# Performance work log

Measured on AMD Instinct MI355X. Metric: run time of the kernel, lower is better.

Reference implementation:

```python
import jax, jax.numpy as jnp
import numpy as np


def setup_inputs() -> dict:
    key = jax.random.key(0)
    k1, = jax.random.split(key, 1)
    bs, A, C, H, W = 32, 3, 80, 64, 64
    inp = jax.random.normal(k1, (bs, A * (5 + C), H, W), dtype=jnp.float32)
    anchors = jnp.asarray([[116.0, 90.0], [156.0, 198.0], [373.0, 326.0]], dtype=jnp.float32)
    return {"input": inp, "anchors": anchors, "image_h": 512, "image_w": 512}


def reference(input, anchors, image_h, image_w):
    bs, ch, H, W = input.shape
    A = anchors.shape[0]
    attrs = ch // A            # 5 + num_classes
    C = attrs - 5
    stride_h = jnp.float32(image_h) / H
    stride_w = jnp.float32(image_w) / W

    # (bs, A, attrs, H, W) -> (bs, A, H, W, attrs)
    p = input.reshape(bs, A, attrs, H, W).transpose(0, 1, 3, 4, 2)

    xy = jax.nn.sigmoid(p[..., 0:2])              # (bs, A, H, W, 2)
    wh_raw = p[..., 2:4]
    conf = jax.nn.sigmoid(p[..., 4:5])
    pred_cls = jax.nn.sigmoid(p[..., 5:])

    grid_x = jnp.arange(W, dtype=jnp.float32)             # column index
    grid_y = jnp.arange(H, dtype=jnp.float32)[:, None]    # row index
    grid = jnp.stack(jnp.broadcast_arrays(grid_x, grid_y * jnp.ones((H, W), jnp.float32)), -1)
    # grid[..., 0] = grid_x, grid[..., 1] = grid_y; shape (H, W, 2)

    stride = jnp.stack([stride_w, stride_h])              # (2,)
    box_xy = (xy + grid) * stride                          # center, image coords
    box_wh = jnp.exp(wh_raw) * anchors.reshape(1, A, 1, 1, 2)  # anchors NOT scaled by stride (as in source)

    pred_boxes = jnp.concatenate([box_xy, box_wh], axis=-1)   # (bs, A, H, W, 4)

    out = jnp.concatenate(
        [pred_boxes.reshape(bs, -1, 4), conf.reshape(bs, -1, 1), pred_cls.reshape(bs, -1, C)],
        axis=-1,
    )  # (bs, A*H*W, 5+C)
    return out
```

## Files before the change

kernel.cpp:

```cpp
#include <hip/hip_runtime.h>


#define NB    32
#define NA    3
#define ATTRS 85
#define HH    64
#define WW    64
#define HWSZ  (HH * WW)
#define TPW   16
#define TILES_PER_BA (HWSZ / TPW)
#define CHUNKS (ATTRS * (TPW / 4))
#define WAVE_LDS (TPW * ATTRS)

typedef float f32x4 __attribute__((ext_vector_type(4)));

__device__ __forceinline__ float fast_sigmoid(float x) {
    return __builtin_amdgcn_rcpf(1.0f + __expf(-x));
}

__global__ __launch_bounds__(256)
void yolo_decode_kernel(const float* __restrict__ in,
                        const float* __restrict__ anchors,
                        const int* __restrict__ imh,
                        const int* __restrict__ imw,
                        float* __restrict__ out)
{
    __shared__ float lds[4 * WAVE_LDS];

    const int tid  = threadIdx.x;
    const int wid  = tid >> 6;
    const int lane = tid & 63;
    float* __restrict__ wlds = lds + wid * WAVE_LDS;

    const int wtile = blockIdx.x * 4 + wid;
    const int tile  = wtile & (TILES_PER_BA - 1);
    const int ba    = wtile >> 8;
    const int b     = ba / NA;
    const int a     = ba - b * NA;
    const int pos0  = tile * TPW;

    const float stride_w = (float)(*imw) / (float)WW;
    const float stride_h = (float)(*imh) / (float)HH;
    const float aw = anchors[a * 2 + 0];
    const float ah = anchors[a * 2 + 1];

    const float gy  = (float)(pos0 >> 6);
    const int   gx0 = pos0 & (WW - 1);

    const float* __restrict__ src =
        in + (size_t)(b * (NA * ATTRS) + a * ATTRS) * HWSZ + pos0;

    f32x4 v[6];
#pragma unroll
    for (int k = 0; k < 5; ++k) {
        const int i = k * 64 + lane;
        v[k] = *(const f32x4*)(src + (i >> 2) * HWSZ + (i & 3) * 4);
    }
    const bool tail = (lane < CHUNKS - 5 * 64);
    if (tail) {
        const int i = 5 * 64 + lane;
        v[5] = *(const f32x4*)(src + (i >> 2) * HWSZ + (i & 3) * 4);
    }

#pragma unroll
    for (int k = 0; k < 6; ++k) {
        if (k == 5 && !tail) break;
        const int i    = k * 64 + lane;
        const int attr = i >> 2;
        const int p4   = i & 3;
        float x[4] = {v[k].x, v[k].y, v[k].z, v[k].w};
        float r[4];
        if (attr >= 4) {
#pragma unroll
            for (int j = 0; j < 4; ++j)
                r[j] = fast_sigmoid(x[j]);
        } else if (attr == 0) {
#pragma unroll
            for (int j = 0; j < 4; ++j)
                r[j] = (fast_sigmoid(x[j]) + (float)(gx0 + p4 * 4 + j)) * stride_w;
        } else if (attr == 1) {
#pragma unroll
            for (int j = 0; j < 4; ++j)
                r[j] = (fast_sigmoid(x[j]) + gy) * stride_h;
        } else if (attr == 2) {
#pragma unroll
            for (int j = 0; j < 4; ++j)
                r[j] = __expf(x[j]) * aw;
        } else {
#pragma unroll
            for (int j = 0; j < 4; ++j)
                r[j] = __expf(x[j]) * ah;
        }
#pragma unroll
        for (int j = 0; j < 4; ++j)
            wlds[(p4 * 4 + j) * ATTRS + attr] = r[j];
    }

    float* __restrict__ dst =
        out + ((size_t)ba * HWSZ + pos0) * ATTRS;
#pragma unroll
    for (int k = 0; k < 5; ++k) {
        const int i = k * 64 + lane;
        *(f32x4*)(dst + i * 4) = *(const f32x4*)(wlds + i * 4);
    }
    if (tail) {
        const int i = 5 * 64 + lane;
        *(f32x4*)(dst + i * 4) = *(const f32x4*)(wlds + i * 4);
    }
}

extern "C" void kernel_launch(void* const* d_in, const int* in_sizes, int n_in,
                              void* d_out, int out_size, void* d_ws, size_t ws_size,
                              hipStream_t stream) {
    const float* in      = (const float*)d_in[0];
    const float* anchors = (const float*)d_in[1];
    const int*   imh     = (const int*)d_in[2];
    const int*   imw     = (const int*)d_in[3];
    float* out = (float*)d_out;

    const int nwaves  = NB * NA * TILES_PER_BA;
    const int nblocks = nwaves / 4;
    yolo_decode_kernel<<<nblocks, 256, 0, stream>>>(in, anchors, imh, imw, out);
}
```

Baseline: 45.43 us.

## Process a full row per wave with register double-buffered prefetch

Each wave now handles an entire 64-pixel row as four 16-pixel tiles instead of a single tile. While the current tile is decoded and written out through LDS, the loads for the next tile are issued into a second register buffer. The aim is to hide global-load latency and spread the per-wave setup over more work. In exchange the grid has a quarter as many blocks and register pressure roughly doubles, which may reduce how much memory parallelism comes from wave count.

```diff
diff --git a/kernel.cpp b/kernel.cpp
--- a/kernel.cpp
+++ b/kernel.cpp
@@ -8,7 +8,6 @@
 #define WW    64
 #define HWSZ  (HH * WW)
 #define TPW   16
-#define TILES_PER_BA (HWSZ / TPW)
 #define CHUNKS (ATTRS * (TPW / 4))
 #define WAVE_LDS (TPW * ATTRS)
 
@@ -32,80 +31,100 @@
     const int lane = tid & 63;
     float* __restrict__ wlds = lds + wid * WAVE_LDS;
 
-    const int wtile = blockIdx.x * 4 + wid;
-    const int tile  = wtile & (TILES_PER_BA - 1);
-    const int ba    = wtile >> 8;
-    const int b     = ba / NA;
-    const int a     = ba - b * NA;
-    const int pos0  = tile * TPW;
+    const int wjob = blockIdx.x * 4 + wid;
+    const int ba   = wjob >> 6;
+    const int row  = wjob & 63;
+    const int b    = ba / NA;
+    const int a    = ba - b * NA;
 
     const float stride_w = (float)(*imw) / (float)WW;
     const float stride_h = (float)(*imh) / (float)HH;
     const float aw = anchors[a * 2 + 0];
     const float ah = anchors[a * 2 + 1];
-
-    const float gy  = (float)(pos0 >> 6);
-    const int   gx0 = pos0 & (WW - 1);
+    const float gy = (float)row;
 
     const float* __restrict__ src =
-        in + (size_t)(b * (NA * ATTRS) + a * ATTRS) * HWSZ + pos0;
+        in + (size_t)ba * ATTRS * HWSZ + row * WW;
+    float* __restrict__ dstw =
+        out + ((size_t)ba * HWSZ + row * WW) * ATTRS;
 
-    f32x4 v[6];
+    const bool tail = (lane < CHUNKS - 5 * 64);
+
+    f32x4 va[2][6];
+
 #pragma unroll
     for (int k = 0; k < 5; ++k) {
         const int i = k * 64 + lane;
-        v[k] = *(const f32x4*)(src + (i >> 2) * HWSZ + (i & 3) * 4);
+        va[0][k] = *(const f32x4*)(src + (i >> 2) * HWSZ + (i & 3) * 4);
     }
-    const bool tail = (lane < CHUNKS - 5 * 64);
     if (tail) {
         const int i = 5 * 64 + lane;
-        v[5] = *(const f32x4*)(src + (i >> 2) * HWSZ + (i & 3) * 4);
+        va[0][5] = *(const f32x4*)(src + (i >> 2) * HWSZ + (i & 3) * 4);
     }
 
 #pragma unroll
-    for (int k = 0; k < 6; ++k) {
-        if (k == 5 && !tail) break;
-        const int i    = k * 64 + lane;
-        const int attr = i >> 2;
-        const int p4   = i & 3;
-        float x[4] = {v[k].x, v[k].y, v[k].z, v[k].w};
-        float r[4];
-        if (attr >= 4) {
+    for (int t = 0; t < 4; ++t) {
+        const int cur = t & 1;
+        const int nxt = cur ^ 1;
+
+        if (t < 3) {
+            const float* __restrict__ s2 = src + (t + 1) * TPW;
+#pragma unroll
+            for (int k = 0; k < 5; ++k) {
+                const int i = k * 64 + lane;
+                va[nxt][k] = *(const f32x4*)(s2 + (i >> 2) * HWSZ + (i & 3) * 4);
+            }
+            if (tail) {
+                const int i = 5 * 64 + lane;
+                va[nxt][5] = *(const f32x4*)(s2 + (i >> 2) * HWSZ + (i & 3) * 4);
+            }
+        }
+
+        const int gx0 = t * TPW;
+#pragma unroll
+        for (int k = 0; k < 6; ++k) {
+            if (k == 5 && !tail) break;
+            const int i    = k * 64 + lane;
+            const int attr = i >> 2;
+            const int p4   = i & 3;
+            float x[4] = {va[cur][k].x, va[cur][k].y, va[cur][k].z, va[cur][k].w};
+            float r[4];
+            if (attr >= 4) {
+#pragma unroll
+                for (int j = 0; j < 4; ++j)
+                    r[j] = fast_sigmoid(x[j]);
+            } else if (attr == 0) {
+#pragma unroll
+                for (int j = 0; j < 4; ++j)
+                    r[j] = (fast_sigmoid(x[j]) + (float)(gx0 + p4 * 4 + j)) * stride_w;
+            } else if (attr == 1) {
+#pragma unroll
+                for (int j = 0; j < 4; ++j)
+                    r[j] = (fast_sigmoid(x[j]) + gy) * stride_h;
+            } else if (attr == 2) {
+#pragma unroll
+                for (int j = 0; j < 4; ++j)
+                    r[j] = __expf(x[j]) * aw;
+            } else {
+#pragma unroll
+                for (int j = 0; j < 4; ++j)
+                    r[j] = __expf(x[j]) * ah;
+            }
 #pragma unroll
             for (int j = 0; j < 4; ++j)
-                r[j] = fast_sigmoid(x[j]);
-        } else if (attr == 0) {
+                wlds[(p4 * 4 + j) * ATTRS + attr] = r[j];
+        }
+
+        float* __restrict__ dst = dstw + t * TPW * ATTRS;
 #pragma unroll
-            for (int j = 0; j < 4; ++j)
-                r[j] = (fast_sigmoid(x[j]) + (float)(gx0 + p4 * 4 + j)) * stride_w;
-        } else if (attr == 1) {
-#pragma unroll
-            for (int j = 0; j < 4; ++j)
-                r[j] = (fast_sigmoid(x[j]) + gy) * stride_h;
-        } else if (attr == 2) {
-#pragma unroll
-            for (int j = 0; j < 4; ++j)
-                r[j] = __expf(x[j]) * aw;
-        } else {
-#pragma unroll
-            for (int j = 0; j < 4; ++j)
-                r[j] = __expf(x[j]) * ah;
+        for (int k = 0; k < 5; ++k) {
+            const int i = k * 64 + lane;
+            *(f32x4*)(dst + i * 4) = *(const f32x4*)(wlds + i * 4);
         }
-#pragma unroll
-        for (int j = 0; j < 4; ++j)
-            wlds[(p4 * 4 + j) * ATTRS + attr] = r[j];
-    }
-
-    float* __restrict__ dst =
-        out + ((size_t)ba * HWSZ + pos0) * ATTRS;
-#pragma unroll
-    for (int k = 0; k < 5; ++k) {
-        const int i = k * 64 + lane;
-        *(f32x4*)(dst + i * 4) = *(const f32x4*)(wlds + i * 4);
-    }
-    if (tail) {
-        const int i = 5 * 64 + lane;
-        *(f32x4*)(dst + i * 4) = *(const f32x4*)(wlds + i * 4);
+        if (tail) {
+            const int i = 5 * 64 + lane;
+            *(f32x4*)(dst + i * 4) = *(const f32x4*)(wlds + i * 4);
+        }
     }
 }
 
@@ -118,7 +137,7 @@
     const int*   imw     = (const int*)d_in[3];
     float* out = (float*)d_out;
 
-    const int nwaves  = NB * NA * TILES_PER_BA;
-    const int nblocks = nwaves / 4;
+    const int njobs   = NB * NA * HH;
+    const int nblocks = njobs / 4;
     yolo_decode_kernel<<<nblocks, 256, 0, stream>>>(in, anchors, imh, imw, out);
 }
```

Measured after the change: 52.98 us. +16.6%, slower.
